# Performance work log

Measured on AMD Instinct MI355X. Metric: run time of the kernel, lower is better.

Reference implementation:

```python
import jax, jax.numpy as jnp
import numpy as np

MARGIN = 0.5
EPS = 1e-10


def setup_inputs() -> dict:
    key = jax.random.key(0)
    k1, k2 = jax.random.split(key)
    n, d = 8192, 256
    xs = jax.random.normal(k1, (n, d), dtype=jnp.float32)
    ys = jax.random.randint(k2, (n,), 0, 64, dtype=jnp.int64)
    return {"xs": xs, "ys": ys}


def reference(xs, ys):
    n = xs.shape[0]
    # pairwise squared L2: ||a||^2 + ||b||^2 - 2 a.b  -> [n, n]
    sq = jnp.sum(xs * xs, axis=1)
    dist2 = sq[:, None] + sq[None, :] - 2.0 * (xs @ xs.T)
    dist = jnp.sqrt(jnp.maximum(dist2, EPS))
    # same-label mask (includes diagonal, as in the original)
    mask = (ys[None, :] == ys[:, None]).astype(dist.dtype)  # [n, n]
    pos_cnt = jnp.sum(mask, axis=1)
    neg_cnt = n - pos_cnt
    dist_ap = jnp.sum(dist * mask, axis=1) / pos_cnt
    dist_an = jnp.sum(dist * (1.0 - mask), axis=1) / neg_cnt
    # MarginRankingLoss with y=1: mean(relu(-(dist_an - dist_ap) + margin))
    loss = jnp.mean(jnp.maximum(dist_ap - dist_an + MARGIN, 0.0))
    return loss
```

## Files before the change

kernel.cpp:

```cpp
#include <hip/hip_runtime.h>
#include <math.h>

#define N 8192
#define D 256
#define BK 32
#define TILE 128
#define NB (N / TILE)
#define NBLK (NB * (NB + 1) / 2)

typedef _Float16 half8 __attribute__((ext_vector_type(8)));
typedef float f32x4 __attribute__((ext_vector_type(4)));

constexpr float MARGIN = 0.5f;
constexpr float EPS_F  = 1e-10f;

__device__ inline void load_lds16(const void* g, void* l) {
    __builtin_amdgcn_global_load_lds(
        (const __attribute__((address_space(1))) void*)g,
        (__attribute__((address_space(3))) void*)l, 16, 0, 0);
}

__global__ void prep_kernel(const float* __restrict__ xs,
                            const int* __restrict__ ys_raw,
                            _Float16* __restrict__ x16, float* __restrict__ sq,
                            int* __restrict__ lbl, int* __restrict__ hist16,
                            float* __restrict__ sums, float* __restrict__ out) {
    const int tid = threadIdx.x;
    const int rb  = blockIdx.x;

    {
        const int r   = tid >> 4;
        const int c16 = tid & 15;
        const int row = rb * 16 + r;

        const float4* src = (const float4*)xs + (size_t)row * (D / 4) + c16 * 4;
        const float4 v0 = src[0], v1 = src[1], v2 = src[2], v3 = src[3];

        half8 h0 = { (_Float16)v0.x, (_Float16)v0.y, (_Float16)v0.z, (_Float16)v0.w,
                     (_Float16)v1.x, (_Float16)v1.y, (_Float16)v1.z, (_Float16)v1.w };
        half8 h1 = { (_Float16)v2.x, (_Float16)v2.y, (_Float16)v2.z, (_Float16)v2.w,
                     (_Float16)v3.x, (_Float16)v3.y, (_Float16)v3.z, (_Float16)v3.w };

        _Float16* dst = x16 + (size_t)row * D + c16 * 16;
        *(half8*)dst       = h0;
        *(half8*)(dst + 8) = h1;

        float s = v0.x*v0.x + v0.y*v0.y + v0.z*v0.z + v0.w*v0.w
                + v1.x*v1.x + v1.y*v1.y + v1.z*v1.z + v1.w*v1.w
                + v2.x*v2.x + v2.y*v2.y + v2.z*v2.z + v2.w*v2.w
                + v3.x*v3.x + v3.y*v3.y + v3.z*v3.z + v3.w*v3.w;
#pragma unroll
        for (int off = 1; off < 16; off <<= 1) s += __shfl_xor(s, off);
        if (c16 == 0) sq[row] = s;
    }

    if (rb < 16) {
        __shared__ int bad_s;
        __shared__ int lh[64];
        const int base = rb * 512;
        if (tid == 0) bad_s = 0;
        if (tid < 64) lh[tid] = 0;
        __syncthreads();
        int bad = 0;
        for (int i = tid; i < 512; i += 256) bad |= (ys_raw[2 * (base + i) + 1] != 0);
        if (bad) atomicOr(&bad_s, 1);
        __syncthreads();
        const bool is64 = (bad_s == 0);
        for (int i = tid; i < 512; i += 256) {
            const int v = is64 ? ys_raw[2 * (base + i)] : ys_raw[base + i];
            lbl[base + i] = v;
            atomicAdd(&lh[v & 63], 1);
        }
        __syncthreads();
        if (tid < 64) hist16[rb * 64 + tid] = lh[tid];
    }

    if (rb >= 16 && rb < 48) {
        const int off = (rb - 16) * 512 + tid;
        sums[off]       = 0.f;
        sums[off + 256] = 0.f;
    }
    if (rb == 48 && tid == 0) out[0] = 0.f;
}

__global__ __launch_bounds__(256, 3) void pair_kernel(
    const _Float16* __restrict__ x16, const int* __restrict__ lbl,
    const float* __restrict__ sq,
    float* __restrict__ sum_same, float* __restrict__ sum_all) {

    __shared__ _Float16 As[3][TILE * BK];
    __shared__ _Float16 Bs[3][TILE * BK];

    const int t = (blockIdx.x % 8) * (NBLK / 8) + blockIdx.x / 8;

    int bj = (int)((sqrtf(8.f * (float)t + 1.f) - 1.f) * 0.5f);
    while ((bj + 1) * (bj + 2) / 2 <= t) ++bj;
    while (bj * (bj + 1) / 2 > t) --bj;
    const int bi    = t - bj * (bj + 1) / 2;
    const bool diag = (bi == bj);
    const int i0 = bi * TILE;
    const int j0 = bj * TILE;

    const int tid  = threadIdx.x;
    const int w    = tid >> 6;
    const int lane = tid & 63;
    const int wm   = w >> 1;
    const int wn   = w & 1;
    const int cl   = lane & 15;
    const int g    = lane >> 4;

    f32x4 acc[4][4];
#pragma unroll
    for (int a = 0; a < 4; ++a)
#pragma unroll
        for (int b = 0; b < 4; ++b) acc[a][b] = (f32x4){0.f, 0.f, 0.f, 0.f};

    const int c0 = w * 64 + lane;
    const int r0 = c0 >> 2, kc0 = c0 & 3;
    const int c1 = 256 + c0;
    const int r1 = c1 >> 2, kc1 = c1 & 3;

#define STAGE(buf, k0)                                                          \
    do {                                                                        \
        load_lds16(x16 + (size_t)(i0 + r0) * D + (k0) + kc0 * 8,                \
                   &As[buf][(size_t)(w * 64) * 8]);                             \
        load_lds16(x16 + (size_t)(j0 + r0) * D + (k0) + kc0 * 8,                \
                   &Bs[buf][(size_t)(w * 64) * 8]);                             \
        load_lds16(x16 + (size_t)(i0 + r1) * D + (k0) + kc1 * 8,                \
                   &As[buf][(size_t)(256 + w * 64) * 8]);                       \
        load_lds16(x16 + (size_t)(j0 + r1) * D + (k0) + kc1 * 8,                \
                   &Bs[buf][(size_t)(256 + w * 64) * 8]);                       \
    } while (0)

    STAGE(0, 0);
    STAGE(1, BK);

    const int colbase = j0 + wn * 64;
    float sqj_[4];
    int   yj_[4];

#pragma unroll
    for (int t8 = 0; t8 < 8; ++t8) {
        const int cur = t8 % 3;
        if (t8 < 6) STAGE((t8 + 2) % 3, (t8 + 2) * BK);

        if (t8 < 6)       asm volatile("s_waitcnt vmcnt(8)" ::: "memory");
        else if (t8 == 6) asm volatile("s_waitcnt vmcnt(4)" ::: "memory");
        else              asm volatile("s_waitcnt vmcnt(0)" ::: "memory");
        __builtin_amdgcn_s_barrier();

        if (t8 == 7) {
#pragma unroll
            for (int nf = 0; nf < 4; ++nf) {
                const int c = colbase + nf * 16 + cl;
                sqj_[nf] = sq[c];
                yj_[nf]  = lbl[c];
            }
        }

        half8 af[4], bf[4];
#pragma unroll
        for (int mf = 0; mf < 4; ++mf)
            af[mf] = *(const half8*)&As[cur][(wm * 64 + mf * 16 + cl) * BK + g * 8];
#pragma unroll
        for (int nf = 0; nf < 4; ++nf)
            bf[nf] = *(const half8*)&Bs[cur][(wn * 64 + nf * 16 + cl) * BK + g * 8];

        __builtin_amdgcn_s_setprio(1);
#pragma unroll
        for (int mf = 0; mf < 4; ++mf)
#pragma unroll
            for (int nf = 0; nf < 4; ++nf)
                acc[mf][nf] = __builtin_amdgcn_mfma_f32_16x16x32_f16(
                    af[mf], bf[nf], acc[mf][nf], 0, 0, 0);
        __builtin_amdgcn_s_setprio(0);

        __builtin_amdgcn_s_barrier();
    }
#undef STAGE

    const int rowbase = i0 + wm * 64;

    float cs_all[4], cs_same[4];
#pragma unroll
    for (int nf = 0; nf < 4; ++nf) { cs_all[nf] = 0.f; cs_same[nf] = 0.f; }

#pragma unroll
    for (int b = 0; b < 2; ++b) {
        float rs_all[8], rs_same[8];
#pragma unroll
        for (int e = 0; e < 8; ++e) { rs_all[e] = 0.f; rs_same[e] = 0.f; }

#pragma unroll
        for (int mh = 0; mh < 2; ++mh) {
            const int mf = 2 * b + mh;
#pragma unroll
            for (int r = 0; r < 4; ++r) {
                const int row   = rowbase + mf * 16 + g * 4 + r;
                const float sqi = sq[row];
                const int   yi  = lbl[row];
#pragma unroll
                for (int nf = 0; nf < 4; ++nf) {
                    float d2   = sqi + sqj_[nf] - 2.f * acc[mf][nf][r];
                    float dist = __builtin_amdgcn_sqrtf(fmaxf(d2, EPS_F));
                    if (diag) {
                        const int col = colbase + nf * 16 + cl;
                        if (row == col) dist = 1e-5f;
                    }
                    const float dm = (yi == yj_[nf]) ? dist : 0.f;
                    cs_all[nf] += dist;
                    cs_same[nf] += dm;
                    rs_all[mh * 4 + r] += dist;
                    rs_same[mh * 4 + r] += dm;
                }
            }
        }

        if (!diag) {
#define RSTEP(h, mask, bit)                                                     \
            {                                                                   \
                const bool hi = (cl >> (bit)) & 1;                              \
                _Pragma("unroll")                                               \
                for (int j = 0; j < (h); ++j) {                                 \
                    float sa_ = hi ? rs_all[j] : rs_all[j + (h)];               \
                    float ka_ = hi ? rs_all[j + (h)] : rs_all[j];               \
                    rs_all[j] = ka_ + __shfl_xor(sa_, (mask));                  \
                    float ss_ = hi ? rs_same[j] : rs_same[j + (h)];             \
                    float ks_ = hi ? rs_same[j + (h)] : rs_same[j];             \
                    rs_same[j] = ks_ + __shfl_xor(ss_, (mask));                 \
                }                                                               \
            }
            RSTEP(4, 8, 3)
            RSTEP(2, 4, 2)
            RSTEP(1, 2, 1)
#undef RSTEP
            rs_all[0]  += __shfl_xor(rs_all[0], 1);
            rs_same[0] += __shfl_xor(rs_same[0], 1);

            const int e    = cl >> 1;
            const int rrow = rowbase + (2 * b + (e >> 2)) * 16 + g * 4 + (e & 3);
            if (!(cl & 1)) {
                atomicAdd(&sum_all[rrow],  rs_all[0]);
                atomicAdd(&sum_same[rrow], rs_same[0]);
            }
        }
    }

    {
        const bool hi1 = (g >> 1) & 1;
#pragma unroll
        for (int j = 0; j < 2; ++j) {
            float sa_ = hi1 ? cs_all[j] : cs_all[j + 2];
            float ka_ = hi1 ? cs_all[j + 2] : cs_all[j];
            cs_all[j] = ka_ + __shfl_xor(sa_, 32);
            float ss_ = hi1 ? cs_same[j] : cs_same[j + 2];
            float ks_ = hi1 ? cs_same[j + 2] : cs_same[j];
            cs_same[j] = ks_ + __shfl_xor(ss_, 32);
        }
        const bool hi0 = g & 1;
        {
            float sa_ = hi0 ? cs_all[0] : cs_all[1];
            float ka_ = hi0 ? cs_all[1] : cs_all[0];
            cs_all[0] = ka_ + __shfl_xor(sa_, 16);
            float ss_ = hi0 ? cs_same[0] : cs_same[1];
            float ks_ = hi0 ? cs_same[1] : cs_same[0];
            cs_same[0] = ks_ + __shfl_xor(ss_, 16);
        }
        const int ccol = colbase + g * 16 + cl;
        atomicAdd(&sum_all[ccol],  cs_all[0]);
        atomicAdd(&sum_same[ccol], cs_same[0]);
    }
}

__global__ void finalize_kernel(const float* __restrict__ sum_same,
                                const float* __restrict__ sum_all,
                                const int* __restrict__ lbl,
                                const int* __restrict__ hist16,
                                float* __restrict__ out) {
    __shared__ int lh[64];
    __shared__ float wsums[4];
    const int tid = threadIdx.x;
    if (tid < 64) {
        int h = 0;
#pragma unroll
        for (int b = 0; b < 16; ++b) h += hist16[b * 64 + tid];
        lh[tid] = h;
    }
    __syncthreads();

    const int row = blockIdx.x * 256 + tid;
    const float cnt = (float)lh[lbl[row]];
    const float ss  = sum_same[row];
    const float sa  = sum_all[row];
    const float ap  = ss / cnt;
    const float an  = (sa - ss) / ((float)N - cnt);
    float local = fmaxf(ap - an + MARGIN, 0.f);

#pragma unroll
    for (int off = 32; off > 0; off >>= 1) local += __shfl_down(local, off);
    const int lane = tid & 63, wave = tid >> 6;
    if (lane == 0) wsums[wave] = local;
    __syncthreads();
    if (tid == 0)
        atomicAdd(out, (wsums[0] + wsums[1] + wsums[2] + wsums[3]) / (float)N);
}

extern "C" void kernel_launch(void* const* d_in, const int* in_sizes, int n_in,
                              void* d_out, int out_size, void* d_ws, size_t ws_size,
                              hipStream_t stream) {
    const float* xs     = (const float*)d_in[0];
    const int*   ys_raw = (const int*)d_in[1];

    float* ws       = (float*)d_ws;
    float* sum_same = ws;
    float* sum_all  = ws + N;
    float* sqv      = ws + 2 * N;
    int*   lbl      = (int*)(ws + 3 * N);
    int*   hist16   = (int*)(ws + 4 * N);
    _Float16* x16   = (_Float16*)(ws + 4 * N + 1024);

    prep_kernel<<<N / 16, 256, 0, stream>>>(xs, ys_raw, x16, sqv, lbl, hist16,
                                            sum_same, (float*)d_out);

    pair_kernel<<<NBLK, 256, 0, stream>>>(x16, lbl, sqv, sum_same, sum_all);

    finalize_kernel<<<32, 256, 0, stream>>>(sum_same, sum_all, lbl, hist16,
                                            (float*)d_out);
}
```

Measured before the change: 51.58 us.

## Process two adjacent column tiles per block with a continuous K pipeline

Each workgroup now handles a strip of up to two consecutive upper-triangular 128x128 tiles sharing the same row block, giving 1056 blocks instead of 2080. The triple-buffered LDS load pipeline runs straight across both panels, so the second tile's loads overlap the first tile's epilogue, and the final barrier is skipped. This reduces per-block launch and pipeline-fill overhead and the tail of the triangular grid. The cost is half as many blocks for load balancing, a longer live range for the pipeline, and the A-row tile is still reloaded per panel rather than reused.

```diff
diff --git a/kernel.cpp b/kernel.cpp
--- a/kernel.cpp
+++ b/kernel.cpp
@@ -6,7 +6,7 @@
 #define BK 32
 #define TILE 128
 #define NB (N / TILE)
-#define NBLK (NB * (NB + 1) / 2)
+#define NSTRIP 1056
 
 typedef _Float16 half8 __attribute__((ext_vector_type(8)));
 typedef float f32x4 __attribute__((ext_vector_type(4)));
@@ -91,15 +91,19 @@
     __shared__ _Float16 As[3][TILE * BK];
     __shared__ _Float16 Bs[3][TILE * BK];
 
-    const int t = (blockIdx.x % 8) * (NBLK / 8) + blockIdx.x / 8;
-
-    int bj = (int)((sqrtf(8.f * (float)t + 1.f) - 1.f) * 0.5f);
-    while ((bj + 1) * (bj + 2) / 2 <= t) ++bj;
-    while (bj * (bj + 1) / 2 > t) --bj;
-    const int bi    = t - bj * (bj + 1) / 2;
-    const bool diag = (bi == bj);
-    const int i0 = bi * TILE;
-    const int j0 = bj * TILE;
+    int rem = (blockIdx.x % 8) * (NSTRIP / 8) + blockIdx.x / 8;
+
+    int bi = 0;
+    for (;;) {
+        const int ns = (65 - bi) >> 1;
+        if (rem < ns) break;
+        rem -= ns;
+        ++bi;
+    }
+    const int bj0   = bi + 2 * rem;
+    const int npan  = (bj0 == 63) ? 1 : 2;
+    const int total = npan * 8;
+    const int i0    = bi * TILE;
 
     const int tid  = threadIdx.x;
     const int w    = tid >> 6;
@@ -109,167 +113,188 @@
     const int cl   = lane & 15;
     const int g    = lane >> 4;
 
-    f32x4 acc[4][4];
-#pragma unroll
-    for (int a = 0; a < 4; ++a)
-#pragma unroll
-        for (int b = 0; b < 4; ++b) acc[a][b] = (f32x4){0.f, 0.f, 0.f, 0.f};
+    const int rowbase = i0 + wm * 64;
 
     const int c0 = w * 64 + lane;
     const int r0 = c0 >> 2, kc0 = c0 & 3;
     const int c1 = 256 + c0;
     const int r1 = c1 >> 2, kc1 = c1 & 3;
 
-#define STAGE(buf, k0)                                                          \
+#define STAGE(buf, jbase, k0)                                                   \
     do {                                                                        \
         load_lds16(x16 + (size_t)(i0 + r0) * D + (k0) + kc0 * 8,                \
                    &As[buf][(size_t)(w * 64) * 8]);                             \
-        load_lds16(x16 + (size_t)(j0 + r0) * D + (k0) + kc0 * 8,                \
+        load_lds16(x16 + (size_t)((jbase) + r0) * D + (k0) + kc0 * 8,           \
                    &Bs[buf][(size_t)(w * 64) * 8]);                             \
         load_lds16(x16 + (size_t)(i0 + r1) * D + (k0) + kc1 * 8,                \
                    &As[buf][(size_t)(256 + w * 64) * 8]);                       \
-        load_lds16(x16 + (size_t)(j0 + r1) * D + (k0) + kc1 * 8,                \
+        load_lds16(x16 + (size_t)((jbase) + r1) * D + (k0) + kc1 * 8,           \
                    &Bs[buf][(size_t)(256 + w * 64) * 8]);                       \
     } while (0)
 
-    STAGE(0, 0);
-    STAGE(1, BK);
-
-    const int colbase = j0 + wn * 64;
+    STAGE(0, bj0 * TILE, 0);
+    STAGE(1, bj0 * TILE, BK);
+
     float sqj_[4];
     int   yj_[4];
-
-#pragma unroll
-    for (int t8 = 0; t8 < 8; ++t8) {
-        const int cur = t8 % 3;
-        if (t8 < 6) STAGE((t8 + 2) % 3, (t8 + 2) * BK);
-
-        if (t8 < 6)       asm volatile("s_waitcnt vmcnt(8)" ::: "memory");
-        else if (t8 == 6) asm volatile("s_waitcnt vmcnt(4)" ::: "memory");
-        else              asm volatile("s_waitcnt vmcnt(0)" ::: "memory");
-        __builtin_amdgcn_s_barrier();
-
-        if (t8 == 7) {
+#pragma unroll
+    for (int nf = 0; nf < 4; ++nf) {
+        const int c = bj0 * TILE + wn * 64 + nf * 16 + cl;
+        sqj_[nf] = sq[c];
+        yj_[nf]  = lbl[c];
+    }
+
+#pragma unroll 2
+    for (int p = 0; p < 2; ++p) {
+        if (p == 1 && npan == 1) break;
+        const int  bj      = bj0 + p;
+        const int  j0p     = bj * TILE;
+        const bool diagp   = (bj == bi);
+        const int  colbase = j0p + wn * 64;
+
+        f32x4 acc[4][4];
+#pragma unroll
+        for (int a = 0; a < 4; ++a)
+#pragma unroll
+            for (int b = 0; b < 4; ++b) acc[a][b] = (f32x4){0.f, 0.f, 0.f, 0.f};
+
+#pragma unroll
+        for (int ks = 0; ks < 8; ++ks) {
+            const int it  = p * 8 + ks;
+            const int cur = it % 3;
+            const int u   = it + 2;
+
+            if (u < total) {
+                const int pu  = u >> 3;
+                const int k0n = (u & 7) * BK;
+                STAGE(u % 3, (bj0 + pu) * TILE, k0n);
+            }
+
+            if (it + 2 < total)      asm volatile("s_waitcnt vmcnt(8)" ::: "memory");
+            else if (it + 1 < total) asm volatile("s_waitcnt vmcnt(4)" ::: "memory");
+            else                     asm volatile("s_waitcnt vmcnt(0)" ::: "memory");
+            __builtin_amdgcn_s_barrier();
+
+            half8 af[4], bf[4];
+#pragma unroll
+            for (int mf = 0; mf < 4; ++mf)
+                af[mf] = *(const half8*)&As[cur][(wm * 64 + mf * 16 + cl) * BK + g * 8];
+#pragma unroll
+            for (int nf = 0; nf < 4; ++nf)
+                bf[nf] = *(const half8*)&Bs[cur][(wn * 64 + nf * 16 + cl) * BK + g * 8];
+
+            __builtin_amdgcn_s_setprio(1);
+#pragma unroll
+            for (int mf = 0; mf < 4; ++mf)
+#pragma unroll
+                for (int nf = 0; nf < 4; ++nf)
+                    acc[mf][nf] = __builtin_amdgcn_mfma_f32_16x16x32_f16(
+                        af[mf], bf[nf], acc[mf][nf], 0, 0, 0);
+            __builtin_amdgcn_s_setprio(0);
+
+            if (it + 1 < total) __builtin_amdgcn_s_barrier();
+        }
+
+        float cs_all[4], cs_same[4];
+#pragma unroll
+        for (int nf = 0; nf < 4; ++nf) { cs_all[nf] = 0.f; cs_same[nf] = 0.f; }
+
+#pragma unroll
+        for (int b = 0; b < 2; ++b) {
+            float rs_all[8], rs_same[8];
+#pragma unroll
+            for (int e = 0; e < 8; ++e) { rs_all[e] = 0.f; rs_same[e] = 0.f; }
+
+#pragma unroll
+            for (int mh = 0; mh < 2; ++mh) {
+                const int mf = 2 * b + mh;
+#pragma unroll
+                for (int r = 0; r < 4; ++r) {
+                    const int row   = rowbase + mf * 16 + g * 4 + r;
+                    const float sqi = sq[row];
+                    const int   yi  = lbl[row];
+#pragma unroll
+                    for (int nf = 0; nf < 4; ++nf) {
+                        float d2   = sqi + sqj_[nf] - 2.f * acc[mf][nf][r];
+                        float dist = __builtin_amdgcn_sqrtf(fmaxf(d2, EPS_F));
+                        if (diagp) {
+                            const int col = colbase + nf * 16 + cl;
+                            if (row == col) dist = 1e-5f;
+                        }
+                        const float dm = (yi == yj_[nf]) ? dist : 0.f;
+                        cs_all[nf] += dist;
+                        cs_same[nf] += dm;
+                        rs_all[mh * 4 + r] += dist;
+                        rs_same[mh * 4 + r] += dm;
+                    }
+                }
+            }
+
+            if (!diagp) {
+#define RSTEP(h, mask, bit)                                                     \
+                {                                                               \
+                    const bool hi = (cl >> (bit)) & 1;                          \
+                    _Pragma("unroll")                                           \
+                    for (int j = 0; j < (h); ++j) {                             \
+                        float sa_ = hi ? rs_all[j] : rs_all[j + (h)];           \
+                        float ka_ = hi ? rs_all[j + (h)] : rs_all[j];           \
+                        rs_all[j] = ka_ + __shfl_xor(sa_, (mask));              \
+                        float ss_ = hi ? rs_same[j] : rs_same[j + (h)];         \
+                        float ks_ = hi ? rs_same[j + (h)] : rs_same[j];         \
+                        rs_same[j] = ks_ + __shfl_xor(ss_, (mask));             \
+                    }                                                           \
+                }
+                RSTEP(4, 8, 3)
+                RSTEP(2, 4, 2)
+                RSTEP(1, 2, 1)
+#undef RSTEP
+                rs_all[0]  += __shfl_xor(rs_all[0], 1);
+                rs_same[0] += __shfl_xor(rs_same[0], 1);
+
+                const int e    = cl >> 1;
+                const int rrow = rowbase + (2 * b + (e >> 2)) * 16 + g * 4 + (e & 3);
+                if (!(cl & 1)) {
+                    atomicAdd(&sum_all[rrow],  rs_all[0]);
+                    atomicAdd(&sum_same[rrow], rs_same[0]);
+                }
+            }
+        }
+
+        {
+            const bool hi1 = (g >> 1) & 1;
+#pragma unroll
+            for (int j = 0; j < 2; ++j) {
+                float sa_ = hi1 ? cs_all[j] : cs_all[j + 2];
+                float ka_ = hi1 ? cs_all[j + 2] : cs_all[j];
+                cs_all[j] = ka_ + __shfl_xor(sa_, 32);
+                float ss_ = hi1 ? cs_same[j] : cs_same[j + 2];
+                float ks_ = hi1 ? cs_same[j + 2] : cs_same[j];
+                cs_same[j] = ks_ + __shfl_xor(ss_, 32);
+            }
+            const bool hi0 = g & 1;
+            {
+                float sa_ = hi0 ? cs_all[0] : cs_all[1];
+                float ka_ = hi0 ? cs_all[1] : cs_all[0];
+                cs_all[0] = ka_ + __shfl_xor(sa_, 16);
+                float ss_ = hi0 ? cs_same[0] : cs_same[1];
+                float ks_ = hi0 ? cs_same[1] : cs_same[0];
+                cs_same[0] = ks_ + __shfl_xor(ss_, 16);
+            }
+            const int ccol = colbase + g * 16 + cl;
+            atomicAdd(&sum_all[ccol],  cs_all[0]);
+            atomicAdd(&sum_same[ccol], cs_same[0]);
+        }
+
+        if (p == 0 && npan == 2) {
 #pragma unroll
             for (int nf = 0; nf < 4; ++nf) {
-                const int c = colbase + nf * 16 + cl;
+                const int c = (bj0 + 1) * TILE + wn * 64 + nf * 16 + cl;
                 sqj_[nf] = sq[c];
                 yj_[nf]  = lbl[c];
             }
         }
-
-        half8 af[4], bf[4];
-#pragma unroll
-        for (int mf = 0; mf < 4; ++mf)
-            af[mf] = *(const half8*)&As[cur][(wm * 64 + mf * 16 + cl) * BK + g * 8];
-#pragma unroll
-        for (int nf = 0; nf < 4; ++nf)
-            bf[nf] = *(const half8*)&Bs[cur][(wn * 64 + nf * 16 + cl) * BK + g * 8];
-
-        __builtin_amdgcn_s_setprio(1);
-#pragma unroll
-        for (int mf = 0; mf < 4; ++mf)
-#pragma unroll
-            for (int nf = 0; nf < 4; ++nf)
-                acc[mf][nf] = __builtin_amdgcn_mfma_f32_16x16x32_f16(
-                    af[mf], bf[nf], acc[mf][nf], 0, 0, 0);
-        __builtin_amdgcn_s_setprio(0);
-
-        __builtin_amdgcn_s_barrier();
     }
 #undef STAGE
-
-    const int rowbase = i0 + wm * 64;
-
-    float cs_all[4], cs_same[4];
-#pragma unroll
-    for (int nf = 0; nf < 4; ++nf) { cs_all[nf] = 0.f; cs_same[nf] = 0.f; }
-
-#pragma unroll
-    for (int b = 0; b < 2; ++b) {
-        float rs_all[8], rs_same[8];
-#pragma unroll
-        for (int e = 0; e < 8; ++e) { rs_all[e] = 0.f; rs_same[e] = 0.f; }
-
-#pragma unroll
-        for (int mh = 0; mh < 2; ++mh) {
-            const int mf = 2 * b + mh;
-#pragma unroll
-            for (int r = 0; r < 4; ++r) {
-                const int row   = rowbase + mf * 16 + g * 4 + r;
-                const float sqi = sq[row];
-                const int   yi  = lbl[row];
-#pragma unroll
-                for (int nf = 0; nf < 4; ++nf) {
-                    float d2   = sqi + sqj_[nf] - 2.f * acc[mf][nf][r];
-                    float dist = __builtin_amdgcn_sqrtf(fmaxf(d2, EPS_F));
-                    if (diag) {
-                        const int col = colbase + nf * 16 + cl;
-                        if (row == col) dist = 1e-5f;
-                    }
-                    const float dm = (yi == yj_[nf]) ? dist : 0.f;
-                    cs_all[nf] += dist;
-                    cs_same[nf] += dm;
-                    rs_all[mh * 4 + r] += dist;
-                    rs_same[mh * 4 + r] += dm;
-                }
-            }
-        }
-
-        if (!diag) {
-#define RSTEP(h, mask, bit)                                                     \
-            {                                                                   \
-                const bool hi = (cl >> (bit)) & 1;                              \
-                _Pragma("unroll")                                               \
-                for (int j = 0; j < (h); ++j) {                                 \
-                    float sa_ = hi ? rs_all[j] : rs_all[j + (h)];               \
-                    float ka_ = hi ? rs_all[j + (h)] : rs_all[j];               \
-                    rs_all[j] = ka_ + __shfl_xor(sa_, (mask));                  \
-                    float ss_ = hi ? rs_same[j] : rs_same[j + (h)];             \
-                    float ks_ = hi ? rs_same[j + (h)] : rs_same[j];             \
-                    rs_same[j] = ks_ + __shfl_xor(ss_, (mask));                 \
-                }                                                               \
-            }
-            RSTEP(4, 8, 3)
-            RSTEP(2, 4, 2)
-            RSTEP(1, 2, 1)
-#undef RSTEP
-            rs_all[0]  += __shfl_xor(rs_all[0], 1);
-            rs_same[0] += __shfl_xor(rs_same[0], 1);
-
-            const int e    = cl >> 1;
-            const int rrow = rowbase + (2 * b + (e >> 2)) * 16 + g * 4 + (e & 3);
-            if (!(cl & 1)) {
-                atomicAdd(&sum_all[rrow],  rs_all[0]);
-                atomicAdd(&sum_same[rrow], rs_same[0]);
-            }
-        }
-    }
-
-    {
-        const bool hi1 = (g >> 1) & 1;
-#pragma unroll
-        for (int j = 0; j < 2; ++j) {
-            float sa_ = hi1 ? cs_all[j] : cs_all[j + 2];
-            float ka_ = hi1 ? cs_all[j + 2] : cs_all[j];
-            cs_all[j] = ka_ + __shfl_xor(sa_, 32);
-            float ss_ = hi1 ? cs_same[j] : cs_same[j + 2];
-            float ks_ = hi1 ? cs_same[j + 2] : cs_same[j];
-            cs_same[j] = ks_ + __shfl_xor(ss_, 32);
-        }
-        const bool hi0 = g & 1;
-        {
-            float sa_ = hi0 ? cs_all[0] : cs_all[1];
-            float ka_ = hi0 ? cs_all[1] : cs_all[0];
-            cs_all[0] = ka_ + __shfl_xor(sa_, 16);
-            float ss_ = hi0 ? cs_same[0] : cs_same[1];
-            float ks_ = hi0 ? cs_same[1] : cs_same[0];
-            cs_same[0] = ks_ + __shfl_xor(ss_, 16);
-        }
-        const int ccol = colbase + g * 16 + cl;
-        atomicAdd(&sum_all[ccol],  cs_all[0]);
-        atomicAdd(&sum_same[ccol], cs_same[0]);
-    }
 }
 
 __global__ void finalize_kernel(const float* __restrict__ sum_same,
@@ -322,7 +347,7 @@
     prep_kernel<<<N / 16, 256, 0, stream>>>(xs, ys_raw, x16, sqv, lbl, hist16,
                                             sum_same, (float*)d_out);
 
-    pair_kernel<<<NBLK, 256, 0, stream>>>(x16, lbl, sqv, sum_same, sum_all);
+    pair_kernel<<<NSTRIP, 256, 0, stream>>>(x16, lbl, sqv, sum_same, sum_all);
 
     finalize_kernel<<<32, 256, 0, stream>>>(sum_same, sum_all, lbl, hist16,
                                             (float*)d_out);
```

Result: slower. 85.01 us (+64.8%).
